# Kernel optimization log

Measured on AMD Instinct MI355X. Metric: run time of the kernel, lower is better.

The kernel has to match this reference:

```python
import jax, jax.numpy as jnp
import numpy as np

IN_SIZE = 224
KERNEL = 5
STRIDE = 1
IN_CH = 16
OUT_CH = 64
LAMB = 5.0
LR = 0.005
GAMMA = 0.99
EPS_ = 0.01
NH = (IN_SIZE - KERNEL) // STRIDE + 1          # 220 output positions per side
NB_TILES = NH * NH                              # 48400 tiles


def setup_inputs() -> dict:
    key = jax.random.key(0)
    k1, k2 = jax.random.split(key)
    x = jax.random.normal(k1, (1, IN_CH, IN_SIZE, IN_SIZE), dtype=jnp.float32)
    # torch.nn.init.uniform_(param, a=0, b=1)
    W = jax.random.uniform(k2, (OUT_CH, IN_CH, KERNEL, KERNEL), dtype=jnp.float32)
    exp_avg = jnp.zeros((OUT_CH,), dtype=jnp.float32)
    return {"x": x, "W": W, "exp_avg": exp_avg, "clamped": 0}


def _inhibition(out):
    out = jax.nn.relu(out)
    m = jnp.max(out, axis=1, keepdims=True)     # max over channel dim
    out = out / (m + 1e-9)
    return out ** LAMB


def _flatten_input(x):
    # mirrors x.unfold(2,k,s).unfold(3,k,s) -> [T, C*k*k] with (C, kh, kw) ordering
    starts = jnp.arange(NH) * STRIDE
    rows = starts[:, None] + jnp.arange(KERNEL)  # [NH, K]
    p = x[0][:, rows]                            # [C, NH, K, W]
    p = p[:, :, :, rows]                         # [C, NH, K, NH, K]
    p = p.transpose(1, 3, 0, 2, 4)               # [NH, NH, C, K, K]
    return p.reshape(NB_TILES, -1)               # [T, D]


def reference(x, W, exp_avg, clamped):
    # forward conv + inhibition
    out = jax.lax.conv_general_dilated(
        x, W, (STRIDE, STRIDE), 'VALID',
        dimension_numbers=('NCHW', 'OIHW', 'NCHW'))
    out = _inhibition(out)                       # [1, O, NH, NH]

    # Hebbian FullyOrthogonal update (no-grad buffer update in the original)
    y = out[0].transpose(1, 2, 0).reshape(-1, OUT_CH)   # [T, O]
    xf = _flatten_input(x)                               # [T, D]
    Wf = W.reshape(OUT_CH, -1)                           # [O, D]
    # mean_t( lr * (y_t (x) x_t - y_t (x) (y_t W)) ) = lr/T * (Y^T X - (Y^T Y) W)
    yty = y.T @ y                                        # [O, O]
    avg_delta = (LR / NB_TILES) * (y.T @ xf - yty @ Wf)  # [O, D]
    Wnew = jax.nn.relu(Wf + avg_delta).reshape(OUT_CH, IN_CH, KERNEL, KERNEL)
    exp_new = GAMMA * exp_avg + (1.0 - GAMMA) * jnp.mean(y, axis=0)

    # weight decay scaling
    A = exp_new / jnp.mean(exp_new)
    gfp = EPS_ * jnp.tanh(-EPS_ * (A - 1.0)) + 1.0
    gfn = 1.0 / gfp
    pos = jnp.where(Wnew > 0, Wnew, 0.0) * gfp.reshape(-1, 1, 1, 1)
    neg = jnp.where(Wnew < 0, Wnew, 0.0) * gfn.reshape(-1, 1, 1, 1)
    Wfinal = pos + neg
    return out, Wfinal, exp_new
```

## Files before the change

kernel.cpp:

```cpp
#include <hip/hip_runtime.h>
#include <stdint.h>

#define IN_SIZE 224
#define KER 5
#define IN_CH 16
#define OUT_CH 64
#define NH 220
#define NB_TILES (NH * NH)
#define XCH (IN_SIZE * IN_SIZE)
#define OUT_PLANE NB_TILES
#define KP2 51200
#define XS 52224
#define XTROWS 50304
#define LR_OVER_NB ((float)(0.005 / 48400.0))
#define GAMMA_F 0.99f
#define ONE_MINUS_GAMMA 0.01f
#define EPS_F 0.01f

#define NCHUNK 64
#define CK 800
#define PSTRIDE (64 * 512)

typedef __attribute__((ext_vector_type(8))) short short8;
typedef __attribute__((ext_vector_type(4))) float floatx4;

__device__ inline uint16_t f2bf(float f) {
    uint32_t u = __float_as_uint(f);
    return (uint16_t)((u + 0x7FFFu + ((u >> 16) & 1u)) >> 16);
}
__device__ inline float bf2f(uint16_t h) { return __uint_as_float((uint32_t)h << 16); }

__global__ __launch_bounds__(256) void xcast_kernel(const float* __restrict__ x,
                                                    uint16_t* __restrict__ xs,
                                                    uint16_t* __restrict__ yb,
                                                    uint16_t* __restrict__ ones) {
    int t = blockIdx.x * 256 + threadIdx.x;
    const int perq = XS / 4;
    if (t < 5 * 16 * perq) {
        int kj = t / (16 * perq);
        int rem = t - kj * (16 * perq);
        int c = rem / perq;
        int q = (rem - c * perq) * 4;
        int base = c * XCH;
        ushort4 o;
        int i0 = q + kj;     o.x = f2bf(x[base + (i0 < XCH ? i0 : XCH - 1)]);
        int i1 = q + kj + 1; o.y = f2bf(x[base + (i1 < XCH ? i1 : XCH - 1)]);
        int i2 = q + kj + 2; o.z = f2bf(x[base + (i2 < XCH ? i2 : XCH - 1)]);
        int i3 = q + kj + 3; o.w = f2bf(x[base + (i3 < XCH ? i3 : XCH - 1)]);
        *(ushort4*)(xs + (kj * 16 + c) * XS + q) = o;
    }
    ushort4 z = {0, 0, 0, 0};
    if (t < 64 * 480) {
        int r = t / 480, q = (t - r * 480) * 4;
        *(ushort4*)(yb + r * KP2 + 49280 + q) = z;
    }
    if (t < 64 * 220) {
        int o = t / 220, i = t - o * 220;
        *(ushort4*)(yb + o * KP2 + i * 224 + 220) = z;
    }
    if (t < 12816) {
        ushort4 o1 = {0x3F80, 0x3F80, 0x3F80, 0x3F80};
        ((ushort4*)ones)[t] = o1;
    }
}

__global__ __launch_bounds__(256) void prep_kernel(const float* __restrict__ x,
                                                   uint16_t* __restrict__ xth,
                                                   uint16_t* __restrict__ xtl,
                                                   const float* __restrict__ W,
                                                   uint16_t* __restrict__ wrh,
                                                   uint16_t* __restrict__ wrl) {
    int b = blockIdx.x;
    if (b < 197) {
        int addr = b * 256 + threadIdx.x;
        if (addr >= XTROWS) return;
        uint32_t dh[8], dl[8];
        if (addr < XCH) {
#pragma unroll
            for (int q = 0; q < 8; q++) {
                float v0 = x[(2 * q) * XCH + addr];
                float v1 = x[(2 * q + 1) * XCH + addr];
                uint16_t h0 = f2bf(v0), h1 = f2bf(v1);
                uint16_t l0 = f2bf(v0 - bf2f(h0)), l1 = f2bf(v1 - bf2f(h1));
                dh[q] = (uint32_t)h0 | ((uint32_t)h1 << 16);
                dl[q] = (uint32_t)l0 | ((uint32_t)l1 << 16);
            }
        } else {
#pragma unroll
            for (int q = 0; q < 8; q++) { dh[q] = 0u; dl[q] = 0u; }
        }
        *(uint4*)(xth + addr * 16) = make_uint4(dh[0], dh[1], dh[2], dh[3]);
        *(uint4*)(xth + addr * 16 + 8) = make_uint4(dh[4], dh[5], dh[6], dh[7]);
        *(uint4*)(xtl + addr * 16) = make_uint4(dl[0], dl[1], dl[2], dl[3]);
        *(uint4*)(xtl + addr * 16 + 8) = make_uint4(dl[4], dl[5], dl[6], dl[7]);
    } else {
        int idx = (b - 197) * 256 + threadIdx.x;
        if (idx >= 13 * 4 * 64 * 8) return;
        int j = idx & 7;
        int lane = (idx >> 3) & 63;
        int ocg = (idx >> 9) & 3;
        int t = idx >> 11;
        int k = (lane >> 4) * 8 + j;
        int s = k >> 4, c = k & 15;
        int oc = 16 * ocg + (lane & 15);
        int tap = 2 * t + s;
        float v = (tap < 25) ? W[oc * 400 + c * 25 + tap] : 0.f;
        uint16_t h = f2bf(v);
        wrh[idx] = h;
        wrl[idx] = f2bf(v - bf2f(h));
    }
}

__global__ __launch_bounds__(256) void conv_inhib_kernel(const uint16_t* __restrict__ xth,
                                                         const uint16_t* __restrict__ xtl,
                                                         const uint16_t* __restrict__ wrh,
                                                         const uint16_t* __restrict__ wrl,
                                                         float* __restrict__ out,
                                                         uint16_t* __restrict__ yb) {
    const int lane = threadIdx.x & 63;
    const int w = threadIdx.x >> 6;
    const int l15 = lane & 15;
    const int quad = lane >> 4;
    const int P0 = blockIdx.x * 64;
    const int c0 = (quad & 1) * 8;
    const int sq = quad >> 1;

    floatx4 acc[4];
#pragma unroll
    for (int g = 0; g < 4; g++) acc[g] = (floatx4){0.f, 0.f, 0.f, 0.f};

#pragma unroll
    for (int t = 0; t < 13; t++) {
        short8 ah = *(const short8*)(wrh + ((t * 4 + w) * 64 + lane) * 8);
        short8 al = *(const short8*)(wrl + ((t * 4 + w) * 64 + lane) * 8);
        const int tap0 = 2 * t, tap1 = 2 * t + 1;
        const int o0 = (tap0 / 5) * 224 + (tap0 % 5);
        const int o1 = (tap1 <= 24) ? (tap1 / 5) * 224 + (tap1 % 5) : 0;
        const int off = sq ? o1 : o0;
#pragma unroll
        for (int g = 0; g < 4; g++) {
            int P = P0 + 16 * g + l15;
            short8 bh = *(const short8*)(xth + (P + off) * 16 + c0);
            short8 bl = *(const short8*)(xtl + (P + off) * 16 + c0);
            acc[g] = __builtin_amdgcn_mfma_f32_16x16x32_bf16(ah, bh, acc[g], 0, 0, 0);
            acc[g] = __builtin_amdgcn_mfma_f32_16x16x32_bf16(ah, bl, acc[g], 0, 0, 0);
            acc[g] = __builtin_amdgcn_mfma_f32_16x16x32_bf16(al, bh, acc[g], 0, 0, 0);
        }
    }

    __shared__ float wmax[4][64];
    float pmax[4];
#pragma unroll
    for (int g = 0; g < 4; g++) {
        float mx = fmaxf(fmaxf(acc[g][0], acc[g][1]), fmaxf(acc[g][2], acc[g][3]));
        mx = fmaxf(mx, 0.f);
        mx = fmaxf(mx, __shfl_xor(mx, 16));
        mx = fmaxf(mx, __shfl_xor(mx, 32));
        pmax[g] = mx;
    }
    if (quad == 0) {
#pragma unroll
        for (int g = 0; g < 4; g++) wmax[w][g * 16 + l15] = pmax[g];
    }
    __syncthreads();

#pragma unroll
    for (int g = 0; g < 4; g++) {
        int P = P0 + 16 * g + l15;
        int i = P / 224;
        int j = P - i * 224;
        bool valid = j < NH;
        float mx = fmaxf(fmaxf(wmax[0][g * 16 + l15], wmax[1][g * 16 + l15]),
                         fmaxf(wmax[2][g * 16 + l15], wmax[3][g * 16 + l15]));
        float inv = 1.f / (mx + 1e-9f);
#pragma unroll
        for (int r = 0; r < 4; r++) {
            float tv = fmaxf(acc[g][r], 0.f) * inv;
            float t2 = tv * tv;
            tv = t2 * t2 * tv;
            if (valid) {
                int oc = 16 * w + quad * 4 + r;
                out[oc * OUT_PLANE + i * NH + j] = tv;
                yb[oc * KP2 + P] = f2bf(tv);
            }
        }
    }
}

__global__ __launch_bounds__(256) void gemm_kernel(const uint16_t* __restrict__ yb,
                                                   const uint16_t* __restrict__ xs,
                                                   const uint16_t* __restrict__ ones,
                                                   float* __restrict__ Mpart) {
    __shared__ uint16_t As[2][64 * 40];
    __shared__ uint16_t Bs[2][64 * 40];
    const int tid = threadIdx.x;
    const int lane = tid & 63;
    const int w = tid >> 6;
    const int l15 = lane & 15;
    const int quad = lane >> 4;
    const int kg = quad * 8;
    const int b = blockIdx.x;
    const int xcd = b & 7;
    const int t8 = b >> 3;
    const int ntile = t8 & 7;
    const int chunk = xcd + 8 * (t8 >> 3);
    const int k0 = chunk * CK;

    const int sr = tid >> 2;
    const int sseg = (tid & 3) * 8;
    const uint16_t* pa = yb + sr * KP2 + k0 + sseg;

    int n_g = ntile * 64 + sr;
    const uint16_t* pbase;
    if (n_g < 400) {
        int c = n_g / 25;
        int r = n_g - 25 * c;
        int ki = r / 5;
        int kj = r - 5 * ki;
        pbase = xs + (kj * 16 + c) * XS + ki * 224;
    } else if (n_g < 464) {
        pbase = yb + (n_g - 400) * KP2;
    } else if (n_g == 464) {
        pbase = ones;
    } else {
        pbase = yb;
    }
    const uint16_t* pb = pbase + k0 + sseg;

    floatx4 acc[4];
#pragma unroll
    for (int i = 0; i < 4; i++) acc[i] = (floatx4){0.f, 0.f, 0.f, 0.f};

    uint4 ra = *(const uint4*)pa;
    uint4 rb = *(const uint4*)pb;

    for (int s = 0; s < 25; s++) {
        const int p = s & 1;
        *(uint4*)&As[p][sr * 40 + sseg] = ra;
        *(uint4*)&Bs[p][sr * 40 + sseg] = rb;
        __syncthreads();
        if (s + 1 < 25) {
            pa += 32;
            pb += 32;
            ra = *(const uint4*)pa;
            rb = *(const uint4*)pb;
        }
        short8 af = *(const short8*)&As[p][(16 * w + l15) * 40 + kg];
#pragma unroll
        for (int ng = 0; ng < 4; ng++) {
            short8 bf = *(const short8*)&Bs[p][(16 * ng + l15) * 40 + kg];
            acc[ng] = __builtin_amdgcn_mfma_f32_16x16x32_bf16(af, bf, acc[ng], 0, 0, 0);
        }
        __syncthreads();
    }

    float* dst = Mpart + chunk * PSTRIDE;
#pragma unroll
    for (int ng = 0; ng < 4; ng++) {
        int col = ntile * 64 + ng * 16 + l15;
        if (col < 465) {
#pragma unroll
            for (int r = 0; r < 4; r++)
                dst[(16 * w + quad * 4 + r) * 512 + col] = acc[ng][r];
        }
    }
}

__global__ __launch_bounds__(256) void reduce_kernel(const float* __restrict__ Mpart,
                                                     float* __restrict__ M,
                                                     float* __restrict__ yty,
                                                     float* __restrict__ colsum) {
    int e = blockIdx.x * 256 + threadIdx.x;
    float s = 0.f;
#pragma unroll 8
    for (int ch = 0; ch < NCHUNK; ch++) s += Mpart[ch * PSTRIDE + e];
    int row = e >> 9, col = e & 511;
    if (col < 400) M[row * 400 + col] = s;
    else if (col < 464) yty[row * 64 + (col - 400)] = s;
    else if (col == 464) colsum[row] = s;
}

__global__ __launch_bounds__(256) void finalize_w_kernel(const float* __restrict__ W,
                                                         const float* __restrict__ yty,
                                                         const float* __restrict__ M,
                                                         const float* __restrict__ colsum,
                                                         const float* __restrict__ exp_avg,
                                                         float* __restrict__ Wout,
                                                         float* __restrict__ expout) {
    __shared__ float gfps[OUT_CH];
    if (threadIdx.x < OUT_CH) {
        int o = threadIdx.x;
        float e = GAMMA_F * exp_avg[o] + ONE_MINUS_GAMMA * (colsum[o] / (float)NB_TILES);
        float s = e;
        for (int off = 32; off; off >>= 1) s += __shfl_down(s, off);
        s = __shfl(s, 0);
        float A = e / (s / (float)OUT_CH);
        gfps[o] = EPS_F * tanhf(-EPS_F * (A - 1.f)) + 1.f;
        if (blockIdx.x == 0) expout[o] = e;
    }
    __syncthreads();
    int idx = blockIdx.x * 256 + threadIdx.x;
    int o = idx / 400;
    int q = idx - o * 400;
    float dot = 0.f;
#pragma unroll 8
    for (int k = 0; k < OUT_CH; k++) dot = fmaf(yty[o * 64 + k], W[k * 400 + q], dot);
    float w = W[idx] + LR_OVER_NB * (M[idx] - dot);
    w = fmaxf(w, 0.f);
    float gp = gfps[o];
    float pos = (w > 0.f ? w : 0.f) * gp;
    float neg = (w < 0.f ? w : 0.f) / gp;
    Wout[idx] = pos + neg;
}

extern "C" void kernel_launch(void* const* d_in, const int* in_sizes, int n_in,
                              void* d_out, int out_size, void* d_ws, size_t ws_size,
                              hipStream_t stream) {
    const float* x = (const float*)d_in[0];
    const float* W = (const float*)d_in[1];
    const float* exp_avg = (const float*)d_in[2];
    float* out = (float*)d_out;

    float* wsf = (float*)d_ws;
    float* colsum = wsf;
    float* M = wsf + 64;
    float* yty = wsf + 25664;
    float* Mpart = wsf + 29760;
    uint16_t* xth = (uint16_t*)Mpart;
    uint16_t* xtl = xth + XTROWS * 16;
    uint16_t* wrh = xtl + XTROWS * 16;
    uint16_t* wrl = wrh + 26624;
    uint16_t* ybf = (uint16_t*)(wsf + 29760 + NCHUNK * PSTRIDE);
    uint16_t* xsb = ybf + OUT_CH * KP2;
    uint16_t* ones = xsb + 5 * 16 * XS;

    float* Wout = out + OUT_CH * OUT_PLANE;
    float* expout = Wout + OUT_CH * IN_CH * KER * KER;

    xcast_kernel<<<4080, 256, 0, stream>>>(x, xsb, ybf, ones);
    prep_kernel<<<301, 256, 0, stream>>>(x, xth, xtl, W, wrh, wrl);
    conv_inhib_kernel<<<770, 256, 0, stream>>>(xth, xtl, wrh, wrl, out, ybf);
    gemm_kernel<<<512, 256, 0, stream>>>(ybf, xsb, ones, Mpart);
    reduce_kernel<<<128, 256, 0, stream>>>(Mpart, M, yty, colsum);
    finalize_w_kernel<<<100, 256, 0, stream>>>(W, yty, M, colsum, exp_avg, Wout, expout);
}
```

Measured before the change: 119.3 us.

## Merge xcast into prep kernel and fold partial reduction into finalize

Merges the bf16 cast/zero-fill kernel with the prep kernel into a single launch dispatched by block range. Removes the separate reduce kernel: finalize now sums the 64 chunk partials directly for its M element, the yty rows it needs (staged in shared memory), and the column sums. This cuts two kernel launches and the intermediate M/yty/colsum round trip. In exchange every finalize block redundantly reduces colsum and runs with only 100 blocks.

```diff
diff --git a/kernel.cpp b/kernel.cpp
--- a/kernel.cpp
+++ b/kernel.cpp
@@ -30,49 +30,47 @@
 }
 __device__ inline float bf2f(uint16_t h) { return __uint_as_float((uint32_t)h << 16); }
 
-__global__ __launch_bounds__(256) void xcast_kernel(const float* __restrict__ x,
-                                                    uint16_t* __restrict__ xs,
-                                                    uint16_t* __restrict__ yb,
-                                                    uint16_t* __restrict__ ones) {
-    int t = blockIdx.x * 256 + threadIdx.x;
-    const int perq = XS / 4;
-    if (t < 5 * 16 * perq) {
-        int kj = t / (16 * perq);
-        int rem = t - kj * (16 * perq);
-        int c = rem / perq;
-        int q = (rem - c * perq) * 4;
-        int base = c * XCH;
-        ushort4 o;
-        int i0 = q + kj;     o.x = f2bf(x[base + (i0 < XCH ? i0 : XCH - 1)]);
-        int i1 = q + kj + 1; o.y = f2bf(x[base + (i1 < XCH ? i1 : XCH - 1)]);
-        int i2 = q + kj + 2; o.z = f2bf(x[base + (i2 < XCH ? i2 : XCH - 1)]);
-        int i3 = q + kj + 3; o.w = f2bf(x[base + (i3 < XCH ? i3 : XCH - 1)]);
-        *(ushort4*)(xs + (kj * 16 + c) * XS + q) = o;
-    }
-    ushort4 z = {0, 0, 0, 0};
-    if (t < 64 * 480) {
-        int r = t / 480, q = (t - r * 480) * 4;
-        *(ushort4*)(yb + r * KP2 + 49280 + q) = z;
-    }
-    if (t < 64 * 220) {
-        int o = t / 220, i = t - o * 220;
-        *(ushort4*)(yb + o * KP2 + i * 224 + 220) = z;
-    }
-    if (t < 12816) {
-        ushort4 o1 = {0x3F80, 0x3F80, 0x3F80, 0x3F80};
-        ((ushort4*)ones)[t] = o1;
-    }
-}
-
 __global__ __launch_bounds__(256) void prep_kernel(const float* __restrict__ x,
+                                                   uint16_t* __restrict__ xs,
+                                                   uint16_t* __restrict__ yb,
+                                                   uint16_t* __restrict__ ones,
                                                    uint16_t* __restrict__ xth,
                                                    uint16_t* __restrict__ xtl,
                                                    const float* __restrict__ W,
                                                    uint16_t* __restrict__ wrh,
                                                    uint16_t* __restrict__ wrl) {
-    int b = blockIdx.x;
-    if (b < 197) {
-        int addr = b * 256 + threadIdx.x;
+    int blk = blockIdx.x;
+    if (blk < 4080) {
+        int t = blk * 256 + threadIdx.x;
+        const int perq = XS / 4;
+        if (t < 5 * 16 * perq) {
+            int kj = t / (16 * perq);
+            int rem = t - kj * (16 * perq);
+            int c = rem / perq;
+            int q = (rem - c * perq) * 4;
+            int base = c * XCH;
+            ushort4 o;
+            int i0 = q + kj;     o.x = f2bf(x[base + (i0 < XCH ? i0 : XCH - 1)]);
+            int i1 = q + kj + 1; o.y = f2bf(x[base + (i1 < XCH ? i1 : XCH - 1)]);
+            int i2 = q + kj + 2; o.z = f2bf(x[base + (i2 < XCH ? i2 : XCH - 1)]);
+            int i3 = q + kj + 3; o.w = f2bf(x[base + (i3 < XCH ? i3 : XCH - 1)]);
+            *(ushort4*)(xs + (kj * 16 + c) * XS + q) = o;
+        }
+        ushort4 z = {0, 0, 0, 0};
+        if (t < 64 * 480) {
+            int r = t / 480, q = (t - r * 480) * 4;
+            *(ushort4*)(yb + r * KP2 + 49280 + q) = z;
+        }
+        if (t < 64 * 220) {
+            int o = t / 220, i = t - o * 220;
+            *(ushort4*)(yb + o * KP2 + i * 224 + 220) = z;
+        }
+        if (t < 12816) {
+            ushort4 o1 = {0x3F80, 0x3F80, 0x3F80, 0x3F80};
+            ((ushort4*)ones)[t] = o1;
+        }
+    } else if (blk < 4080 + 197) {
+        int addr = (blk - 4080) * 256 + threadIdx.x;
         if (addr >= XTROWS) return;
         uint32_t dh[8], dl[8];
         if (addr < XCH) {
@@ -94,7 +92,7 @@
         *(uint4*)(xtl + addr * 16) = make_uint4(dl[0], dl[1], dl[2], dl[3]);
         *(uint4*)(xtl + addr * 16 + 8) = make_uint4(dl[4], dl[5], dl[6], dl[7]);
     } else {
-        int idx = (b - 197) * 256 + threadIdx.x;
+        int idx = (blk - 4080 - 197) * 256 + threadIdx.x;
         if (idx >= 13 * 4 * 64 * 8) return;
         int j = idx & 7;
         int lane = (idx >> 3) & 63;
@@ -266,50 +264,58 @@
     }
 }
 
-__global__ __launch_bounds__(256) void reduce_kernel(const float* __restrict__ Mpart,
-                                                     float* __restrict__ M,
-                                                     float* __restrict__ yty,
-                                                     float* __restrict__ colsum) {
-    int e = blockIdx.x * 256 + threadIdx.x;
-    float s = 0.f;
-#pragma unroll 8
-    for (int ch = 0; ch < NCHUNK; ch++) s += Mpart[ch * PSTRIDE + e];
-    int row = e >> 9, col = e & 511;
-    if (col < 400) M[row * 400 + col] = s;
-    else if (col < 464) yty[row * 64 + (col - 400)] = s;
-    else if (col == 464) colsum[row] = s;
-}
-
 __global__ __launch_bounds__(256) void finalize_w_kernel(const float* __restrict__ W,
-                                                         const float* __restrict__ yty,
-                                                         const float* __restrict__ M,
-                                                         const float* __restrict__ colsum,
+                                                         const float* __restrict__ Mpart,
                                                          const float* __restrict__ exp_avg,
                                                          float* __restrict__ Wout,
                                                          float* __restrict__ expout) {
     __shared__ float gfps[OUT_CH];
-    if (threadIdx.x < OUT_CH) {
-        int o = threadIdx.x;
-        float e = GAMMA_F * exp_avg[o] + ONE_MINUS_GAMMA * (colsum[o] / (float)NB_TILES);
+    __shared__ float ytys[2][OUT_CH];
+    const int tid = threadIdx.x;
+    const int bid = blockIdx.x;
+    const int first_o = (bid * 256) / 400;
+
+    if (tid < OUT_CH) {
+        int o = tid;
+        float cs = 0.f;
+#pragma unroll 8
+        for (int ch = 0; ch < NCHUNK; ch++) cs += Mpart[ch * PSTRIDE + o * 512 + 464];
+        float e = GAMMA_F * exp_avg[o] + ONE_MINUS_GAMMA * (cs / (float)NB_TILES);
         float s = e;
         for (int off = 32; off; off >>= 1) s += __shfl_down(s, off);
         s = __shfl(s, 0);
         float A = e / (s / (float)OUT_CH);
         gfps[o] = EPS_F * tanhf(-EPS_F * (A - 1.f)) + 1.f;
-        if (blockIdx.x == 0) expout[o] = e;
+        if (bid == 0) expout[o] = e;
+    }
+    if (tid >= 128) {
+        int t = tid - 128;
+        int orow = first_o + (t >> 6);
+        int k = t & 63;
+        float s = 0.f;
+        if (orow < OUT_CH) {
+#pragma unroll 8
+            for (int ch = 0; ch < NCHUNK; ch++) s += Mpart[ch * PSTRIDE + orow * 512 + 400 + k];
+        }
+        ytys[t >> 6][k] = s;
     }
     __syncthreads();
-    int idx = blockIdx.x * 256 + threadIdx.x;
+
+    int idx = bid * 256 + tid;
     int o = idx / 400;
     int q = idx - o * 400;
+    float Mv = 0.f;
+#pragma unroll 8
+    for (int ch = 0; ch < NCHUNK; ch++) Mv += Mpart[ch * PSTRIDE + o * 512 + q];
+    const float* yrow = ytys[o - first_o];
     float dot = 0.f;
 #pragma unroll 8
-    for (int k = 0; k < OUT_CH; k++) dot = fmaf(yty[o * 64 + k], W[k * 400 + q], dot);
-    float w = W[idx] + LR_OVER_NB * (M[idx] - dot);
-    w = fmaxf(w, 0.f);
+    for (int k = 0; k < OUT_CH; k++) dot = fmaf(yrow[k], W[k * 400 + q], dot);
+    float wv = W[idx] + LR_OVER_NB * (Mv - dot);
+    wv = fmaxf(wv, 0.f);
     float gp = gfps[o];
-    float pos = (w > 0.f ? w : 0.f) * gp;
-    float neg = (w < 0.f ? w : 0.f) / gp;
+    float pos = (wv > 0.f ? wv : 0.f) * gp;
+    float neg = (wv < 0.f ? wv : 0.f) / gp;
     Wout[idx] = pos + neg;
 }
 
@@ -322,9 +328,6 @@
     float* out = (float*)d_out;
 
     float* wsf = (float*)d_ws;
-    float* colsum = wsf;
-    float* M = wsf + 64;
-    float* yty = wsf + 25664;
     float* Mpart = wsf + 29760;
     uint16_t* xth = (uint16_t*)Mpart;
     uint16_t* xtl = xth + XTROWS * 16;
@@ -337,10 +340,8 @@
     float* Wout = out + OUT_CH * OUT_PLANE;
     float* expout = Wout + OUT_CH * IN_CH * KER * KER;
 
-    xcast_kernel<<<4080, 256, 0, stream>>>(x, xsb, ybf, ones);
-    prep_kernel<<<301, 256, 0, stream>>>(x, xth, xtl, W, wrh, wrl);
+    prep_kernel<<<4080 + 197 + 104, 256, 0, stream>>>(x, xsb, ybf, ones, xth, xtl, W, wrh, wrl);
     conv_inhib_kernel<<<770, 256, 0, stream>>>(xth, xtl, wrh, wrl, out, ybf);
     gemm_kernel<<<512, 256, 0, stream>>>(ybf, xsb, ones, Mpart);
-    reduce_kernel<<<128, 256, 0, stream>>>(Mpart, M, yty, colsum);
-    finalize_w_kernel<<<100, 256, 0, stream>>>(W, yty, M, colsum, exp_avg, Wout, expout);
-}
+    finalize_w_kernel<<<100, 256, 0, stream>>>(W, Mpart, exp_avg, Wout, expout);
+}
```

Result: no change. 119.1 us (-0.1%).
